# Optimization experiments

Measured on AMD Instinct MI355X. Metric: run time of the kernel, lower is better.

Reference implementation:

```python
import jax, jax.numpy as jnp
import numpy as np


def setup_inputs() -> dict:
    key = jax.random.key(0)
    k1, k2, k3 = jax.random.split(key, 3)
    B, Cin, H, W = 32, 128, 56, 56
    E, Cout = 8, 128
    x = jax.random.normal(k1, (B, Cin, H, W), dtype=jnp.float32)
    conv_w = jax.random.normal(k2, (E, Cout, Cin, 3, 3), dtype=jnp.float32) * 0.05
    gate_w = jax.random.normal(k3, (E, Cin), dtype=jnp.float32) * 0.05
    gate_b = jnp.zeros((E,), dtype=jnp.float32)
    return {"x": x, "conv_w": conv_w, "gate_w": gate_w, "gate_b": gate_b, "top_k": 2}


def reference(x, conv_w, gate_w, gate_b, top_k):
    # x: [B, Cin, H, W]; conv_w: [E, Cout, Cin, 3, 3]
    E, Cout, Cin, kh, kw = conv_w.shape
    B = x.shape[0]
    # Gate: global average pool -> linear logits over experts
    gap = x.mean(axis=(2, 3))                      # [B, Cin]
    logits = gap @ gate_w.T + gate_b               # [B, E]
    vals, idx = jax.lax.top_k(logits, top_k)       # [B, k]
    w = jax.nn.softmax(vals, axis=-1)              # renormalize over selected experts
    weights = jnp.zeros((B, E), dtype=x.dtype).at[jnp.arange(B)[:, None], idx].set(w)
    # All experts via a single conv with stacked output channels (stride=1, pad=1 == SAME)
    y = jax.lax.conv_general_dilated(
        x, conv_w.reshape(E * Cout, Cin, kh, kw),
        window_strides=(1, 1), padding='SAME',
        dimension_numbers=('NCHW', 'OIHW', 'NCHW'))  # [B, E*Cout, H, W]
    y = y.reshape(B, E, Cout, y.shape[2], y.shape[3])
    out = jnp.einsum('be,bechw->bchw', weights, y)  # sparse-weight combine
    return out, weights
```

## Files before the change

### kernel.cpp

```cpp
#include <hip/hip_runtime.h>
#include <hip/hip_bf16.h>

constexpr int Bn   = 32;
constexpr int CIN  = 128;
constexpr int Hh   = 56;
constexpr int Ww   = 56;
constexpr int HW   = Hh * Ww;
constexpr int COUT = 128;
constexpr int En   = 8;

typedef __attribute__((ext_vector_type(8))) short bf16x8;
typedef __attribute__((ext_vector_type(4))) float f32x4;

struct GateInfo { int e0, e1; float w0, w1; };

constexpr size_t ROWB = 58 * 32 * 2;
constexpr size_t PGB  = 58 * ROWB;

constexpr size_t XP_OFF  = 0;
constexpr size_t XP_SZ   = (size_t)Bn * 4 * PGB;
constexpr size_t WW_OFF  = XP_OFF + XP_SZ;
constexpr size_t WW_SZ   = (size_t)Bn * 9 * COUT * CIN * 2;
constexpr size_t HS_OFF  = WW_OFF + WW_SZ;
constexpr size_t HS_SZ   = (size_t)Bn * Hh * CIN * 4;
constexpr size_t GAP_OFF = HS_OFF + HS_SZ;
constexpr size_t GAP_SZ  = (size_t)Bn * CIN * 4;
constexpr size_t GI_OFF  = GAP_OFF + GAP_SZ;

__device__ inline void gload_lds16(const void* g, void* l) {
    __builtin_amdgcn_global_load_lds(
        (const __attribute__((address_space(1))) unsigned int*)g,
        (__attribute__((address_space(3))) unsigned int*)l, 16, 0, 0);
}

__global__ __launch_bounds__(256) void zero_kernel(char* __restrict__ xpad) {
    char* pl = xpad + (size_t)blockIdx.x * PGB;
    for (int u = threadIdx.x; u < 912; u += 256) {
        size_t off;
        if (u < 232)      off = (size_t)u * 16;
        else if (u < 464) off = 57 * ROWB + (size_t)(u - 232) * 16;
        else {
            int v = u - 464;
            int r = v / 8 + 1, s = (v & 7) >> 2, a = v & 3;
            off = (size_t)r * ROWB + (s ? 57 : 0) * 64 + a * 16;
        }
        *(int4*)(pl + off) = (int4){0, 0, 0, 0};
    }
}

__global__ __launch_bounds__(256) void convert_kernel(const float* __restrict__ x,
        char* __restrict__ xpad, float* __restrict__ hsum) {
    __shared__ float lt[CIN * 57];
    int gid = blockIdx.x;
    int b = gid / Hh, h = gid % Hh;
    const float* xp = x + (size_t)b * CIN * HW + h * Ww;
    for (int u = threadIdx.x; u < CIN * Ww; u += 256) {
        int c = u / Ww, w = u % Ww;
        lt[c * 57 + w] = xp[(size_t)c * HW + w];
    }
    __syncthreads();
    char* dst = xpad + (size_t)b * 4 * PGB + (size_t)(h + 1) * ROWB;
    for (int u = threadIdx.x; u < 896; u += 256) {
        int g = u / 224, r = u % 224, w = r >> 2, a = r & 3;
        bf16x8 pk;
        #pragma unroll
        for (int j = 0; j < 8; j++) {
            __hip_bfloat16 t = __float2bfloat16(lt[(g * 32 + a * 8 + j) * 57 + w]);
            pk[j] = *reinterpret_cast<short*>(&t);
        }
        *(bf16x8*)(dst + (size_t)g * PGB + (size_t)(w + 1) * 64 + a * 16) = pk;
    }
    if (threadIdx.x < CIN) {
        int c = threadIdx.x;
        float s = 0.f;
        #pragma unroll 8
        for (int w = 0; w < Ww; w++) s += lt[c * 57 + w];
        hsum[((size_t)b * Hh + h) * CIN + c] = s;
    }
}

__global__ void gap2_kernel(const float* __restrict__ hsum, float* __restrict__ gap) {
    int t = blockIdx.x * 256 + threadIdx.x;
    int b = t >> 7, c = t & 127;
    float s = 0.f;
    for (int h = 0; h < Hh; h++) s += hsum[((size_t)b * Hh + h) * CIN + c];
    gap[t] = s * (1.f / (float)HW);
}

__global__ void gate_kernel(const float* __restrict__ gap,
                            const float* __restrict__ gate_w,
                            const float* __restrict__ gate_b,
                            float* __restrict__ wout,
                            GateInfo* __restrict__ info) {
    __shared__ float logits[Bn][En];
    __shared__ GateInfo gi[Bn];
    int tid = threadIdx.x;
    int b = tid >> 3, e = tid & 7;
    float s = gate_b[e];
    const float* g = gap + b * CIN;
    const float* w = gate_w + e * CIN;
    #pragma unroll 8
    for (int c = 0; c < CIN; c++) s += g[c] * w[c];
    logits[b][e] = s;
    __syncthreads();
    if (tid < Bn) {
        float v[En];
        #pragma unroll
        for (int k = 0; k < En; k++) v[k] = logits[tid][k];
        int i0 = 0; float m0 = v[0];
        #pragma unroll
        for (int k = 1; k < En; k++) if (v[k] > m0) { m0 = v[k]; i0 = k; }
        int i1 = -1; float m1 = -1e30f;
        #pragma unroll
        for (int k = 0; k < En; k++) if (k != i0 && v[k] > m1) { m1 = v[k]; i1 = k; }
        float ex = expf(m1 - m0);
        float den = 1.f + ex;
        GateInfo t; t.e0 = i0; t.e1 = i1; t.w0 = 1.f / den; t.w1 = ex / den;
        gi[tid] = t;
        info[tid] = t;
    }
    __syncthreads();
    {
        int bb = tid >> 3, ee = tid & 7;
        GateInfo t = gi[bb];
        wout[tid] = (ee == t.e0) ? t.w0 : (ee == t.e1) ? t.w1 : 0.f;
    }
}

__global__ __launch_bounds__(256) void wcomb_kernel(const float* __restrict__ cw,
        const GateInfo* __restrict__ info, __hip_bfloat16* __restrict__ wws) {
    __shared__ __hip_bfloat16 wl[16 * 1152];
    int b = blockIdx.x >> 3, cg = blockIdx.x & 7;
    GateInfo gi = info[b];
    const float* p0 = cw + (size_t)gi.e0 * COUT * CIN * 9 + (size_t)cg * 16 * 1152;
    const float* p1 = cw + (size_t)gi.e1 * COUT * CIN * 9 + (size_t)cg * 16 * 1152;
    for (int u = threadIdx.x; u < 16 * 1152; u += 256)
        wl[u] = __float2bfloat16(gi.w0 * p0[u] + gi.w1 * p1[u]);
    __syncthreads();
    __hip_bfloat16* wo = wws + (size_t)b * 9 * COUT * CIN + (size_t)cg * 16 * CIN;
    for (int u = threadIdx.x; u < 2304; u += 256) {
        int t = u >> 8, rem = u & 255, co = rem >> 4, a = rem & 15;
        bf16x8 pk;
        #pragma unroll
        for (int j = 0; j < 8; j++)
            pk[j] = *reinterpret_cast<short*>(&wl[co * 1152 + (a * 8 + j) * 9 + t]);
        *(bf16x8*)(wo + (size_t)t * COUT * CIN + co * CIN + a * 8) = pk;
    }
}

__global__ __launch_bounds__(256, 3) void conv_mfma(
        const char* __restrict__ xpad,
        const __hip_bfloat16* __restrict__ wws,
        float* __restrict__ out) {
    __shared__ char xs[2][22528];

    int bid = blockIdx.x;
    int xcd = bid & 7, k = bid >> 3;
    int b   = xcd * 4 + k / 28;
    int r2  = k % 28;
    int cb  = r2 / 14, rb = r2 % 14;
    int row0 = rb * 4, cout0 = cb * 64;
    int tid = threadIdx.x, wave = tid >> 6, lane = tid & 63;
    int wm = wave >> 1, wn = wave & 1;
    int l15 = lane & 15, lk = lane >> 4;

    const char* src = xpad + (size_t)b * 4 * PGB + (size_t)row0 * ROWB;

    int bbase[7];
    #pragma unroll
    for (int i = 0; i < 7; i++) {
        int p = wn * 112 + i * 16 + l15;
        bbase[i] = (p / 56) * (int)ROWB + (p % 56) * 64 + lk * 16;
    }

    const __hip_bfloat16* ap = wws + (size_t)b * 9 * COUT * CIN
                             + (size_t)(cout0 + wm * 32 + l15) * CIN + lk * 8;

    f32x4 acc[2][7];
    #pragma unroll
    for (int mt = 0; mt < 2; mt++)
        #pragma unroll
        for (int i = 0; i < 7; i++) acc[mt][i] = (f32x4){0.f, 0.f, 0.f, 0.f};

    #pragma unroll
    for (int i2 = 0; i2 < 6; i2++) {
        int idx = i2 * 4 + wave;
        if (idx < 22)
            gload_lds16(src + idx * 1024 + lane * 16, &xs[0][idx * 1024]);
    }

    for (int g = 0; g < 4; ++g) {
        __syncthreads();
        if (g < 3) {
            const char* s2 = src + (size_t)(g + 1) * PGB;
            #pragma unroll
            for (int i2 = 0; i2 < 6; i2++) {
                int idx = i2 * 4 + wave;
                if (idx < 22)
                    gload_lds16(s2 + idx * 1024 + lane * 16, &xs[(g + 1) & 1][idx * 1024]);
            }
        }
        const char* xb = xs[g & 1];
        const __hip_bfloat16* at0 = ap + g * 32;
        #pragma unroll
        for (int t = 0; t < 9; t++) {
            const int dr = t / 3, dc = t % 3;
            const __hip_bfloat16* at = at0 + (size_t)t * COUT * CIN;
            bf16x8 a0 = *(const bf16x8*)(at);
            bf16x8 a1 = *(const bf16x8*)(at + 16 * CIN);
            const int toff = dr * (int)ROWB + dc * 64;
            #pragma unroll
            for (int i = 0; i < 7; i++) {
                bf16x8 bv = *(const bf16x8*)(xb + bbase[i] + toff);
                acc[0][i] = __builtin_amdgcn_mfma_f32_16x16x32_bf16(a0, bv, acc[0][i], 0, 0, 0);
                acc[1][i] = __builtin_amdgcn_mfma_f32_16x16x32_bf16(a1, bv, acc[1][i], 0, 0, 0);
            }
        }
    }

    float* outb = out + (size_t)b * COUT * HW + row0 * 56;
    #pragma unroll
    for (int mt = 0; mt < 2; mt++) {
        int cbase = cout0 + wm * 32 + mt * 16 + lk * 4;
        #pragma unroll
        for (int i = 0; i < 7; i++) {
            int pp = wn * 112 + i * 16 + l15;
            #pragma unroll
            for (int j = 0; j < 4; j++)
                outb[(size_t)(cbase + j) * HW + pp] = acc[mt][i][j];
        }
    }
}

extern "C" void kernel_launch(void* const* d_in, const int* in_sizes, int n_in,
                              void* d_out, int out_size, void* d_ws, size_t ws_size,
                              hipStream_t stream) {
    const float* x  = (const float*)d_in[0];
    const float* cw = (const float*)d_in[1];
    const float* gw = (const float*)d_in[2];
    const float* gb = (const float*)d_in[3];

    float* out = (float*)d_out;
    char* ws = (char*)d_ws;
    char* xpad           = ws + XP_OFF;
    __hip_bfloat16* wws  = (__hip_bfloat16*)(ws + WW_OFF);
    float* hsum          = (float*)(ws + HS_OFF);
    float* gap           = (float*)(ws + GAP_OFF);
    GateInfo* info       = (GateInfo*)(ws + GI_OFF);
    float* wout = out + (size_t)Bn * COUT * HW;

    zero_kernel   <<<Bn * 4,  256, 0, stream>>>(xpad);
    convert_kernel<<<Bn * Hh, 256, 0, stream>>>(x, xpad, hsum);
    gap2_kernel   <<<16,      256, 0, stream>>>(hsum, gap);
    gate_kernel   <<<1,       256, 0, stream>>>(gap, gw, gb, wout, info);
    wcomb_kernel  <<<Bn * 8,  256, 0, stream>>>(cw, info, wws);
    conv_mfma     <<<896,     256, 0, stream>>>(xpad, wws, out);
}
```

Measured before the change: 178.4 us.

## Enlarge conv tile to all output channels, swizzle LDS layout, prefetch weights

```diff
diff --git a/kernel.cpp b/kernel.cpp
--- a/kernel.cpp
+++ b/kernel.cpp
@@ -14,8 +14,9 @@
 
 struct GateInfo { int e0, e1; float w0, w1; };
 
-constexpr size_t ROWB = 58 * 32 * 2;
+constexpr size_t ROWB = 58 * 64;
 constexpr size_t PGB  = 58 * ROWB;
+constexpr int TAPSTR  = COUT * CIN;
 
 constexpr size_t XP_OFF  = 0;
 constexpr size_t XP_SZ   = (size_t)Bn * 4 * PGB;
@@ -33,21 +34,6 @@
         (__attribute__((address_space(3))) unsigned int*)l, 16, 0, 0);
 }
 
-__global__ __launch_bounds__(256) void zero_kernel(char* __restrict__ xpad) {
-    char* pl = xpad + (size_t)blockIdx.x * PGB;
-    for (int u = threadIdx.x; u < 912; u += 256) {
-        size_t off;
-        if (u < 232)      off = (size_t)u * 16;
-        else if (u < 464) off = 57 * ROWB + (size_t)(u - 232) * 16;
-        else {
-            int v = u - 464;
-            int r = v / 8 + 1, s = (v & 7) >> 2, a = v & 3;
-            off = (size_t)r * ROWB + (s ? 57 : 0) * 64 + a * 16;
-        }
-        *(int4*)(pl + off) = (int4){0, 0, 0, 0};
-    }
-}
-
 __global__ __launch_bounds__(256) void convert_kernel(const float* __restrict__ x,
         char* __restrict__ xpad, float* __restrict__ hsum) {
     __shared__ float lt[CIN * 57];
@@ -68,7 +54,21 @@
             __hip_bfloat16 t = __float2bfloat16(lt[(g * 32 + a * 8 + j) * 57 + w]);
             pk[j] = *reinterpret_cast<short*>(&t);
         }
-        *(bf16x8*)(dst + (size_t)g * PGB + (size_t)(w + 1) * 64 + a * 16) = pk;
+        int pq = (a + ((w + 1) >> 1)) & 3;
+        *(bf16x8*)(dst + (size_t)g * PGB + (size_t)(w + 1) * 64 + pq * 16) = pk;
+    }
+    if (threadIdx.x < 32) {
+        int t = threadIdx.x, g = t >> 3, side = (t >> 2) & 1, q = t & 3;
+        *(int4*)(xpad + (size_t)b * 4 * PGB + (size_t)g * PGB + (size_t)(h + 1) * ROWB
+                 + (side ? 57 : 0) * 64 + q * 16) = (int4){0, 0, 0, 0};
+    }
+    if (h == 0 || h == 55) {
+        int row = (h == 0) ? 0 : 57;
+        char* base = xpad + (size_t)b * 4 * PGB + (size_t)row * ROWB;
+        for (int u = threadIdx.x; u < 928; u += 256) {
+            int g = u / 232, r = u % 232;
+            *(int4*)(base + (size_t)g * PGB + (size_t)r * 16) = (int4){0, 0, 0, 0};
+        }
     }
     if (threadIdx.x < CIN) {
         int c = threadIdx.x;
@@ -148,7 +148,7 @@
     }
 }
 
-__global__ __launch_bounds__(256, 3) void conv_mfma(
+__global__ __launch_bounds__(256, 2) void conv_mfma(
         const char* __restrict__ xpad,
         const __hip_bfloat16* __restrict__ wws,
         float* __restrict__ out) {
@@ -156,37 +156,48 @@
 
     int bid = blockIdx.x;
     int xcd = bid & 7, k = bid >> 3;
-    int b   = xcd * 4 + k / 28;
-    int r2  = k % 28;
-    int cb  = r2 / 14, rb = r2 % 14;
-    int row0 = rb * 4, cout0 = cb * 64;
+    int b   = xcd * 4 + k / 14;
+    int rb  = k % 14;
+    int row0 = rb * 4;
     int tid = threadIdx.x, wave = tid >> 6, lane = tid & 63;
-    int wm = wave >> 1, wn = wave & 1;
+    int cb = wave >> 1, wn = wave & 1;
+    int cout0 = cb * 64;
     int l15 = lane & 15, lk = lane >> 4;
 
     const char* src = xpad + (size_t)b * 4 * PGB + (size_t)row0 * ROWB;
 
-    int bbase[7];
+    int bA[7], bB[7], bC[7];
     #pragma unroll
     for (int i = 0; i < 7; i++) {
         int p = wn * 112 + i * 16 + l15;
-        bbase[i] = (p / 56) * (int)ROWB + (p % 56) * 64 + lk * 16;
-    }
-
-    const __hip_bfloat16* ap = wws + (size_t)b * 9 * COUT * CIN
-                             + (size_t)(cout0 + wm * 32 + l15) * CIN + lk * 8;
-
-    f32x4 acc[2][7];
-    #pragma unroll
-    for (int mt = 0; mt < 2; mt++)
+        int r = p / 56, m = p % 56;
+        int base = r * (int)ROWB + m * 64;
+        bA[i] = base + ((lk + (m >> 1)) & 3) * 16;
+        bB[i] = base + ((lk + (m >> 1) + 1) & 3) * 16;
+        bC[i] = (m & 1) ? bB[i] : bA[i];
+    }
+
+    const __hip_bfloat16* ap = wws + (size_t)b * 9 * TAPSTR
+                             + (size_t)(cout0 + l15) * CIN + lk * 8;
+
+    f32x4 acc[4][7];
+    #pragma unroll
+    for (int mt = 0; mt < 4; mt++)
         #pragma unroll
         for (int i = 0; i < 7; i++) acc[mt][i] = (f32x4){0.f, 0.f, 0.f, 0.f};
 
-    #pragma unroll
-    for (int i2 = 0; i2 < 6; i2++) {
-        int idx = i2 * 4 + wave;
-        if (idx < 22)
-            gload_lds16(src + idx * 1024 + lane * 16, &xs[0][idx * 1024]);
+    bf16x8 areg[3][4];
+    #pragma unroll
+    for (int mt = 0; mt < 4; mt++)
+        areg[0][mt] = *(const bf16x8*)(ap + (size_t)0 * TAPSTR + mt * 16 * CIN);
+    #pragma unroll
+    for (int mt = 0; mt < 4; mt++)
+        areg[1][mt] = *(const bf16x8*)(ap + (size_t)1 * TAPSTR + mt * 16 * CIN);
+
+    #pragma unroll
+    for (int i = 0; i < 6; i++) {
+        int idx = i * 4 + wave;
+        if (idx < 22) gload_lds16(src + idx * 1024 + lane * 16, &xs[0][idx * 1024]);
     }
 
     for (int g = 0; g < 4; ++g) {
@@ -194,34 +205,43 @@
         if (g < 3) {
             const char* s2 = src + (size_t)(g + 1) * PGB;
             #pragma unroll
-            for (int i2 = 0; i2 < 6; i2++) {
-                int idx = i2 * 4 + wave;
-                if (idx < 22)
-                    gload_lds16(s2 + idx * 1024 + lane * 16, &xs[(g + 1) & 1][idx * 1024]);
+            for (int i = 0; i < 6; i++) {
+                int idx = i * 4 + wave;
+                if (idx < 22) gload_lds16(s2 + idx * 1024 + lane * 16, &xs[(g + 1) & 1][idx * 1024]);
             }
         }
         const char* xb = xs[g & 1];
-        const __hip_bfloat16* at0 = ap + g * 32;
         #pragma unroll
         for (int t = 0; t < 9; t++) {
+            {
+                const int tt = (t < 7) ? t + 2 : t - 7;
+                const int gg_add = (t < 7) ? 0 : 1;
+                int gg = g + gg_add;
+                if (gg < 4) {
+                    const __hip_bfloat16* pa = ap + (size_t)tt * TAPSTR + gg * 32;
+                    #pragma unroll
+                    for (int mt = 0; mt < 4; mt++)
+                        areg[(t + 2) % 3][mt] = *(const bf16x8*)(pa + mt * 16 * CIN);
+                }
+            }
             const int dr = t / 3, dc = t % 3;
-            const __hip_bfloat16* at = at0 + (size_t)t * COUT * CIN;
-            bf16x8 a0 = *(const bf16x8*)(at);
-            bf16x8 a1 = *(const bf16x8*)(at + 16 * CIN);
-            const int toff = dr * (int)ROWB + dc * 64;
+            const int imm = dr * (int)ROWB + dc * 64;
             #pragma unroll
             for (int i = 0; i < 7; i++) {
-                bf16x8 bv = *(const bf16x8*)(xb + bbase[i] + toff);
-                acc[0][i] = __builtin_amdgcn_mfma_f32_16x16x32_bf16(a0, bv, acc[0][i], 0, 0, 0);
-                acc[1][i] = __builtin_amdgcn_mfma_f32_16x16x32_bf16(a1, bv, acc[1][i], 0, 0, 0);
+                int boff = (dc == 0) ? bA[i] : (dc == 1) ? bC[i] : bB[i];
+                bf16x8 bv = *(const bf16x8*)(xb + boff + imm);
+                #pragma unroll
+                for (int mt = 0; mt < 4; mt++)
+                    acc[mt][i] = __builtin_amdgcn_mfma_f32_16x16x32_bf16(
+                        areg[t % 3][mt], bv, acc[mt][i], 0, 0, 0);
             }
         }
     }
 
     float* outb = out + (size_t)b * COUT * HW + row0 * 56;
     #pragma unroll
-    for (int mt = 0; mt < 2; mt++) {
-        int cbase = cout0 + wm * 32 + mt * 16 + lk * 4;
+    for (int mt = 0; mt < 4; mt++) {
+        int cbase = cout0 + mt * 16 + lk * 4;
         #pragma unroll
         for (int i = 0; i < 7; i++) {
             int pp = wn * 112 + i * 16 + l15;
@@ -249,10 +269,9 @@
     GateInfo* info       = (GateInfo*)(ws + GI_OFF);
     float* wout = out + (size_t)Bn * COUT * HW;
 
-    zero_kernel   <<<Bn * 4,  256, 0, stream>>>(xpad);
     convert_kernel<<<Bn * Hh, 256, 0, stream>>>(x, xpad, hsum);
     gap2_kernel   <<<16,      256, 0, stream>>>(hsum, gap);
     gate_kernel   <<<1,       256, 0, stream>>>(gap, gw, gb, wout, info);
     wcomb_kernel  <<<Bn * 8,  256, 0, stream>>>(cw, info, wws);
-    conv_mfma     <<<896,     256, 0, stream>>>(xpad, wws, out);
-}
+    conv_mfma     <<<448,     256, 0, stream>>>(xpad, wws, out);
+}
```

After: 170.7 us. -4.3%, faster.
